# Optimization experiments

Hardware: AMD Instinct MI355X
Metric: run time of the kernel (lower is better)

## Reference

```python
import jax, jax.numpy as jnp
import numpy as np

B, C, H, W = 16, 256, 64, 64

def setup_inputs() -> dict:
    key = jax.random.key(0)
    ks = jax.random.split(key, 4)
    scale = 1.0 / np.sqrt(C)
    return {
        "x": jax.random.normal(ks[0], (B, C, H, W), dtype=jnp.float32),
        "w1": jax.random.normal(ks[1], (C, C), dtype=jnp.float32) * scale,
        "b1": jnp.zeros((C,), dtype=jnp.float32),
        "w2": jax.random.normal(ks[2], (C, C), dtype=jnp.float32) * scale,
        "b2": jnp.zeros((C,), dtype=jnp.float32),
        "w3": jax.random.normal(ks[3], (C, C), dtype=jnp.float32) * scale,
        "b3": jnp.zeros((C,), dtype=jnp.float32),
    }

def reference(x, w1, b1, w2, b2, w3, b3):
    b, c, h, w = x.shape
    n = h * w
    # 1x1 convs == per-pixel linear maps over channels; w has shape [C_out, C_in]
    def proj(wt, bias):
        return jnp.einsum('bchw,oc->bohw', x, wt) + bias[None, :, None, None]
    v = proj(w1, b1).reshape(b, c, n).transpose(0, 2, 1)   # [B, N, C]
    q = proj(w2, b2).reshape(b, c, n)                      # [B, C, N]
    k = proj(w3, b3).reshape(b, c, n)                      # [B, C, N]
    weight = jnp.einsum('bcn,bdn->bcd', q, k)              # [B, C, C]
    # global softmax over the entire flattened C*C matrix per batch element
    weight = jax.nn.softmax(weight.reshape(b, -1), axis=1).reshape(b, c, c)
    out = jnp.einsum('bnc,bcd->bdn', v, weight)            # [B, C, N]
    return out.reshape(x.shape)
```

## Files before the change

### kernel.cpp

```cpp
#include <hip/hip_runtime.h>


typedef unsigned short u16;
typedef __attribute__((ext_vector_type(8))) short short8;
typedef __attribute__((ext_vector_type(4))) float floatx4;

__device__ __forceinline__ u16 f2b(float f) {
  union { float f; unsigned int u; } v; v.f = f;
  unsigned int u = v.u;
  return (u16)((u + 0x7fffu + ((u >> 16) & 1u)) >> 16);
}
__device__ __forceinline__ float b2f(u16 h) {
  union { unsigned int u; float f; } v; v.u = ((unsigned int)h) << 16;
  return v.f;
}

__global__ __launch_bounds__(256) void prep_w_kernel(
    const float* __restrict__ w1, const float* __restrict__ w2, const float* __restrict__ w3,
    u16* __restrict__ W1Th, u16* __restrict__ W2h, u16* __restrict__ W2l,
    u16* __restrict__ W3h, u16* __restrict__ W3l) {
  const int blk = blockIdx.x, t = threadIdx.x;
  if (blk < 64) {
    __shared__ float tile[32][33];
    const int e0 = (blk & 7) * 32, c0 = (blk >> 3) * 32;
    const int tx = t & 31, ty = t >> 5;
#pragma unroll
    for (int i = 0; i < 4; ++i)
      tile[ty + i * 8][tx] = w1[(c0 + ty + i * 8) * 256 + e0 + tx];
    __syncthreads();
#pragma unroll
    for (int i = 0; i < 4; ++i)
      W1Th[(e0 + ty + i * 8) * 256 + c0 + tx] = f2b(tile[tx][ty + i * 8]);
  } else {
    const int i = (blk - 64) * 256 + t;
    const int e = i & 0xffff;
    const float f = (i >> 16) ? w3[e] : w2[e];
    u16 h = f2b(f);
    if (i >> 16) { W3h[e] = h; W3l[e] = f2b(f - b2f(h)); }
    else         { W2h[e] = h; W2l[e] = f2b(f - b2f(h)); }
  }
}

__device__ __forceinline__ void stage8(const float4 a, const float4 b,
                                       u16* dH, u16* dL, float& xa) {
  const float f[8] = {a.x, a.y, a.z, a.w, b.x, b.y, b.z, b.w};
  union { u16 h8[8]; uint4 q; } uh, ul;
#pragma unroll
  for (int i = 0; i < 8; ++i) {
    const u16 hi = f2b(f[i]);
    uh.h8[i] = hi;
    ul.h8[i] = f2b(f[i] - b2f(hi));
    xa += f[i];
  }
  *(uint4*)dH = uh.q;
  *(uint4*)dL = ul.q;
}

__global__ __launch_bounds__(512, 2) void gram_kernel(
    const float* __restrict__ x, float* __restrict__ Gp, float* __restrict__ xsum) {
  constexpr int LR = 40;
  __shared__ u16 lH[2][256 * LR], lL[2][256 * LR];
  const int b = blockIdx.x >> 4, s = blockIdx.x & 15;
  const float* Xb = x + (long)b * 1048576 + s * 256;
  const int t = threadIdx.x;
  const int lane = t & 63, wave = t >> 6;
  const int quad = lane >> 4, l16 = lane & 15;
  const int wm = (wave & 1) * 128, wn = (wave >> 1) * 64;
  const int r0 = t >> 2, qc = (t & 3) * 8;
  const int r1 = r0 + 128;
  floatx4 acc[8][4] = {};
  float xa0 = 0.f, xa1 = 0.f;
  float4 p[4];
  p[0] = *(const float4*)(Xb + (long)r0 * 4096 + qc);
  p[1] = *(const float4*)(Xb + (long)r0 * 4096 + qc + 4);
  p[2] = *(const float4*)(Xb + (long)r1 * 4096 + qc);
  p[3] = *(const float4*)(Xb + (long)r1 * 4096 + qc + 4);
  stage8(p[0], p[1], lH[0] + r0 * LR + qc, lL[0] + r0 * LR + qc, xa0);
  stage8(p[2], p[3], lH[0] + r1 * LR + qc, lL[0] + r1 * LR + qc, xa1);
  __syncthreads();
  for (int kb = 0; kb < 8; ++kb) {
    const int cur = kb & 1, nxt = cur ^ 1;
    if (kb < 7) {
      const long kk = (kb + 1) * 32;
      p[0] = *(const float4*)(Xb + (long)r0 * 4096 + kk + qc);
      p[1] = *(const float4*)(Xb + (long)r0 * 4096 + kk + qc + 4);
      p[2] = *(const float4*)(Xb + (long)r1 * 4096 + kk + qc);
      p[3] = *(const float4*)(Xb + (long)r1 * 4096 + kk + qc + 4);
    }
    const u16* cH = lH[cur];
    const u16* cL = lL[cur];
#pragma unroll
    for (int j = 0; j < 4; ++j) {
      const short8 bh = *(const short8*)(cH + (wn + j * 16 + l16) * LR + quad * 8);
      const short8 bl = *(const short8*)(cL + (wn + j * 16 + l16) * LR + quad * 8);
#pragma unroll
      for (int i = 0; i < 8; ++i) {
        const short8 ah = *(const short8*)(cH + (wm + i * 16 + l16) * LR + quad * 8);
        const short8 al = *(const short8*)(cL + (wm + i * 16 + l16) * LR + quad * 8);
        acc[i][j] = __builtin_amdgcn_mfma_f32_16x16x32_bf16(ah, bh, acc[i][j], 0, 0, 0);
        acc[i][j] = __builtin_amdgcn_mfma_f32_16x16x32_bf16(ah, bl, acc[i][j], 0, 0, 0);
        acc[i][j] = __builtin_amdgcn_mfma_f32_16x16x32_bf16(al, bh, acc[i][j], 0, 0, 0);
      }
    }
    if (kb < 7) {
      stage8(p[0], p[1], lH[nxt] + r0 * LR + qc, lL[nxt] + r0 * LR + qc, xa0);
      stage8(p[2], p[3], lH[nxt] + r1 * LR + qc, lL[nxt] + r1 * LR + qc, xa1);
    }
    __syncthreads();
  }
  {
    float v = xa0;
    v += __shfl_xor(v, 1);
    v += __shfl_xor(v, 2);
    if ((t & 3) == 0) atomicAdd(&xsum[b * 256 + r0], v);
    v = xa1;
    v += __shfl_xor(v, 1);
    v += __shfl_xor(v, 2);
    if ((t & 3) == 0) atomicAdd(&xsum[b * 256 + r1], v);
  }
  float* G = Gp + ((long)b * 16 + s) * 65536;
#pragma unroll
  for (int i = 0; i < 8; ++i) {
    const int row0 = wm + i * 16 + quad * 4;
#pragma unroll
    for (int j = 0; j < 4; ++j) {
      const int col = wn + j * 16 + l16;
#pragma unroll
      for (int r = 0; r < 4; ++r)
        G[(long)(row0 + r) * 256 + col] = acc[i][j][r];
    }
  }
}

__global__ void reduce_g_kernel(const float* __restrict__ Gp, u16* __restrict__ Gh,
                                u16* __restrict__ Gl) {
  const long e = (long)blockIdx.x * 256 + threadIdx.x;
  const long base = ((e >> 16) << 20) + (e & 65535);
  float s = 0.f;
#pragma unroll
  for (int i = 0; i < 16; ++i) s += Gp[base + (long)i * 65536];
  u16 h = f2b(s);
  Gh[e] = h;
  Gl[e] = f2b(s - b2f(h));
}

template <bool X3, int EPI>
__global__ __launch_bounds__(256) void gemm_small(
    const u16* __restrict__ Ah, const u16* __restrict__ Al,
    const u16* __restrict__ Bh, const u16* __restrict__ Bl,
    long aBatch, long bBatch, long oBatch,
    float* __restrict__ outF, u16* __restrict__ outH, u16* __restrict__ outL) {
  constexpr int LR = 40;
  __shared__ u16 smem[(X3 ? 4 : 2) * 64 * LR];
  u16* lAh = smem;
  u16* lBh = smem + 64 * LR;
  u16* lAl = X3 ? (smem + 2 * 64 * LR) : nullptr;
  u16* lBl = X3 ? (smem + 3 * 64 * LR) : nullptr;
  const int b = blockIdx.z;
  const int tm = blockIdx.x & 3, tn = blockIdx.x >> 2;
  const u16* Ahb = Ah + (long)b * aBatch + (long)tm * 64 * 256;
  const u16* Bhb = Bh + (long)b * bBatch + (long)tn * 64 * 256;
  const u16* Alb = X3 ? (Al + (long)b * aBatch + (long)tm * 64 * 256) : nullptr;
  const u16* Blb = X3 ? (Bl + (long)b * bBatch + (long)tn * 64 * 256) : nullptr;
  const int t = threadIdx.x;
  const int lane = t & 63, wave = t >> 6;
  const int quad = lane >> 4, l16 = lane & 15;
  const int wm = (wave & 1) * 32, wn = (wave >> 1) * 32;
  const int r = t >> 2, qc = (t & 3) * 8;
  floatx4 acc[2][2] = {};
  for (int kk = 0; kk < 256; kk += 32) {
    __syncthreads();
    *(uint4*)(lAh + r * LR + qc) = *(const uint4*)(Ahb + (long)r * 256 + kk + qc);
    *(uint4*)(lBh + r * LR + qc) = *(const uint4*)(Bhb + (long)r * 256 + kk + qc);
    if (X3) {
      *(uint4*)(lAl + r * LR + qc) = *(const uint4*)(Alb + (long)r * 256 + kk + qc);
      *(uint4*)(lBl + r * LR + qc) = *(const uint4*)(Blb + (long)r * 256 + kk + qc);
    }
    __syncthreads();
    short8 afh[2], bfh[2], afl[2], bfl[2];
#pragma unroll
    for (int i = 0; i < 2; ++i) {
      afh[i] = *(const short8*)(lAh + (wm + i * 16 + l16) * LR + quad * 8);
      bfh[i] = *(const short8*)(lBh + (wn + i * 16 + l16) * LR + quad * 8);
      if (X3) {
        afl[i] = *(const short8*)(lAl + (wm + i * 16 + l16) * LR + quad * 8);
        bfl[i] = *(const short8*)(lBl + (wn + i * 16 + l16) * LR + quad * 8);
      }
    }
#pragma unroll
    for (int i = 0; i < 2; ++i)
#pragma unroll
      for (int j = 0; j < 2; ++j) {
        acc[i][j] = __builtin_amdgcn_mfma_f32_16x16x32_bf16(afh[i], bfh[j], acc[i][j], 0, 0, 0);
        if (X3) {
          acc[i][j] = __builtin_amdgcn_mfma_f32_16x16x32_bf16(afh[i], bfl[j], acc[i][j], 0, 0, 0);
          acc[i][j] = __builtin_amdgcn_mfma_f32_16x16x32_bf16(afl[i], bfh[j], acc[i][j], 0, 0, 0);
        }
      }
  }
  const long obase = (long)b * oBatch;
#pragma unroll
  for (int i = 0; i < 2; ++i) {
    const int mb = tm * 64 + wm + i * 16 + quad * 4;
#pragma unroll
    for (int j = 0; j < 2; ++j) {
      const int n = tn * 64 + wn + j * 16 + l16;
#pragma unroll
      for (int rr = 0; rr < 4; ++rr) {
        const float v = acc[i][j][rr];
        const long idx = obase + (long)(mb + rr) * 256 + n;
        if (EPI == 0) {
          outF[idx] = v;
        } else if (EPI == 1) {
          u16 h = f2b(v);
          outH[idx] = h;
          outL[idx] = f2b(v - b2f(h));
        } else {
          outH[idx] = f2b(v);
        }
      }
    }
  }
}

__global__ __launch_bounds__(256) void gemm_out(
    const u16* __restrict__ Mh, const float* __restrict__ x,
    const float* __restrict__ bb, float* __restrict__ out) {
  constexpr int LR = 40;
  __shared__ u16 lA[128 * LR], lB[128 * LR];
  const int b = blockIdx.z;
  const int tm = blockIdx.x & 1, tn = blockIdx.x >> 1;
  const u16* Ab = Mh + (long)b * 65536;
  const float* Xb = x + (long)b * 1048576 + tn * 128;
  const int t = threadIdx.x;
  const int lane = t & 63, wave = t >> 6;
  const int quad = lane >> 4, l16 = lane & 15;
  const int wm = (wave & 1) * 64, wn = (wave >> 1) * 64;
  const int erp = (t >> 4) * 2;
  const int n0 = (t & 15) * 8;
  floatx4 acc[4][4] = {};
  for (int kk = 0; kk < 256; kk += 32) {
    __syncthreads();
#pragma unroll
    for (int h = 0; h < 2; ++h) {
      const int r = (t >> 2) + h * 64;
      *(uint4*)(lA + r * LR + (t & 3) * 8) =
          *(const uint4*)(Ab + (long)(tm * 128 + r) * 256 + kk + (t & 3) * 8);
    }
    {
      const float4 a0 = *(const float4*)(Xb + (long)(kk + erp) * 4096 + n0);
      const float4 a1 = *(const float4*)(Xb + (long)(kk + erp) * 4096 + n0 + 4);
      const float4 c0 = *(const float4*)(Xb + (long)(kk + erp + 1) * 4096 + n0);
      const float4 c1 = *(const float4*)(Xb + (long)(kk + erp + 1) * 4096 + n0 + 4);
      const float fa[8] = {a0.x, a0.y, a0.z, a0.w, a1.x, a1.y, a1.z, a1.w};
      const float fc[8] = {c0.x, c0.y, c0.z, c0.w, c1.x, c1.y, c1.z, c1.w};
#pragma unroll
      for (int i = 0; i < 8; ++i) {
        const int nl = n0 + i;
        const int sb = (erp >> 3) ^ ((nl >> 4) & 3);
        const unsigned int pk =
            (unsigned int)f2b(fa[i]) | ((unsigned int)f2b(fc[i]) << 16);
        *(unsigned int*)(lB + nl * LR + sb * 8 + (erp & 7)) = pk;
      }
    }
    __syncthreads();
    short8 af[4], bf[4];
#pragma unroll
    for (int i = 0; i < 4; ++i) {
      af[i] = *(const short8*)(lA + (wm + i * 16 + l16) * LR + quad * 8);
      const int n = wn + i * 16 + l16;
      const int rb = quad ^ ((n >> 4) & 3);
      bf[i] = *(const short8*)(lB + n * LR + rb * 8);
    }
#pragma unroll
    for (int i = 0; i < 4; ++i)
#pragma unroll
      for (int j = 0; j < 4; ++j)
        acc[i][j] = __builtin_amdgcn_mfma_f32_16x16x32_bf16(af[i], bf[j], acc[i][j], 0, 0, 0);
  }
  const long obase = (long)b * 1048576;
#pragma unroll
  for (int i = 0; i < 4; ++i) {
    const int mb = tm * 128 + wm + i * 16 + quad * 4;
#pragma unroll
    for (int j = 0; j < 4; ++j) {
      const int n = tn * 128 + wn + j * 16 + l16;
#pragma unroll
      for (int r = 0; r < 4; ++r)
        out[obase + (long)(mb + r) * 4096 + n] = acc[i][j][r] + bb[b * 256 + mb + r];
    }
  }
}

__global__ __launch_bounds__(512) void bias_prep_kernel(
    const float* __restrict__ w2, const float* __restrict__ w3,
    const float* __restrict__ xsum, float* __restrict__ S2, float* __restrict__ S3) {
  __shared__ float xs[256];
  const int b = blockIdx.x, t = threadIdx.x;
  if (t < 256) xs[t] = xsum[b * 256 + t];
  __syncthreads();
  const float* wm = (t < 256) ? w2 : w3;
  const int a = t & 255;
  float s = 0.f;
#pragma unroll 4
  for (int c = 0; c < 256; ++c) s += wm[a * 256 + c] * xs[c];
  if (t < 256) S2[b * 256 + a] = s;
  else         S3[b * 256 + a] = s;
}

__global__ __launch_bounds__(256) void softmax_pass1(
    const float* __restrict__ Lt, const float* __restrict__ S2, const float* __restrict__ S3,
    const float* __restrict__ b2, const float* __restrict__ b3,
    float* __restrict__ bm, float* __restrict__ bs) {
  __shared__ float ls2[256], lb2[256];
  __shared__ float redm[4], reds[4];
  const int b = blockIdx.y, blk = blockIdx.x, t = threadIdx.x;
  ls2[t] = S2[b * 256 + t];
  lb2[t] = b2[t];
  __syncthreads();
  const int fw0 = blk * 2048 + t * 8;
  const int d = fw0 >> 8, a0 = fw0 & 255;
  const float c1 = b3[d];
  const float c0 = S3[b * 256 + d] + 4096.f * c1;
  const long base = (long)b * 65536 + fw0;
  float4 v0 = *(const float4*)(Lt + base);
  float4 v1 = *(const float4*)(Lt + base + 4);
  float v[8] = {v0.x, v0.y, v0.z, v0.w, v1.x, v1.y, v1.z, v1.w};
  float m = -3.4e38f;
#pragma unroll
  for (int i = 0; i < 8; ++i) {
    v[i] += lb2[a0 + i] * c0 + c1 * ls2[a0 + i];
    m = fmaxf(m, v[i]);
  }
  for (int o = 32; o; o >>= 1) m = fmaxf(m, __shfl_xor(m, o));
  const int wid = t >> 6, lane = t & 63;
  if (lane == 0) redm[wid] = m;
  __syncthreads();
  const float bmax = fmaxf(fmaxf(redm[0], redm[1]), fmaxf(redm[2], redm[3]));
  float s = 0.f;
#pragma unroll
  for (int i = 0; i < 8; ++i) s += __expf(v[i] - bmax);
  for (int o = 32; o; o >>= 1) s += __shfl_xor(s, o);
  if (lane == 0) reds[wid] = s;
  __syncthreads();
  if (t == 0) {
    bm[b * 32 + blk] = bmax;
    bs[b * 32 + blk] = reds[0] + reds[1] + reds[2] + reds[3];
  }
}

__global__ __launch_bounds__(256) void softmax_pass3(
    const float* __restrict__ Lt, const float* __restrict__ S2, const float* __restrict__ S3,
    const float* __restrict__ b2, const float* __restrict__ b3,
    const float* __restrict__ bm, const float* __restrict__ bs,
    u16* __restrict__ WTh) {
  __shared__ float ls2[256], lb2[256];
  __shared__ float sM, sInv;
  const int b = blockIdx.y, blk = blockIdx.x, t = threadIdx.x;
  if (t < 64) {
    const float m = (t < 32) ? bm[b * 32 + t] : -3.4e38f;
    float s = (t < 32) ? bs[b * 32 + t] : 0.f;
    float M = m;
    for (int o = 32; o; o >>= 1) M = fmaxf(M, __shfl_xor(M, o));
    s *= __expf(m - M);
    for (int o = 32; o; o >>= 1) s += __shfl_xor(s, o);
    if (t == 0) { sM = M; sInv = 1.0f / s; }
  }
  ls2[t] = S2[b * 256 + t];
  lb2[t] = b2[t];
  __syncthreads();
  const float M = sM, inv = sInv;
  const int fw0 = blk * 2048 + t * 8;
  const int d = fw0 >> 8, a0 = fw0 & 255;
  const float c1 = b3[d];
  const float c0 = S3[b * 256 + d] + 4096.f * c1;
  const long base = (long)b * 65536 + fw0;
  float4 v0 = *(const float4*)(Lt + base);
  float4 v1 = *(const float4*)(Lt + base + 4);
  float v[8] = {v0.x, v0.y, v0.z, v0.w, v1.x, v1.y, v1.z, v1.w};
  union { u16 h[8]; uint4 q; } o;
#pragma unroll
  for (int i = 0; i < 8; ++i) {
    const float vv = v[i] + lb2[a0 + i] * c0 + c1 * ls2[a0 + i];
    o.h[i] = f2b(__expf(vv - M) * inv);
  }
  *(uint4*)(WTh + base) = o.q;
}

__global__ void bb_kernel(const u16* __restrict__ WTh, const float* __restrict__ b1,
                          float* __restrict__ bb) {
  const int b = blockIdx.x, d = threadIdx.x;
  const u16* row = WTh + (long)b * 65536 + d * 256;
  float s = 0.f;
#pragma unroll 4
  for (int c = 0; c < 256; ++c) s += b2f(row[c]) * b1[c];
  bb[b * 256 + d] = s;
}

extern "C" void kernel_launch(void* const* d_in, const int* in_sizes, int n_in,
                              void* d_out, int out_size, void* d_ws, size_t ws_size,
                              hipStream_t stream) {
  const float* x  = (const float*)d_in[0];
  const float* w1 = (const float*)d_in[1];
  const float* b1 = (const float*)d_in[2];
  const float* w2 = (const float*)d_in[3];
  const float* b2 = (const float*)d_in[4];
  const float* w3 = (const float*)d_in[5];
  const float* b3 = (const float*)d_in[6];
  float* out = (float*)d_out;

  char* ws = (char*)d_ws;
  size_t off = 0;
  auto alloc = [&](size_t bytes) {
    void* p = ws + off;
    off += (bytes + 255) & ~(size_t)255;
    return p;
  };
  float* Gp = (float*)alloc(16ull * 16 * 65536 * 4);
  u16* Gh   = (u16*)alloc(16ull * 65536 * 2);
  u16* Gl   = (u16*)alloc(16ull * 65536 * 2);
  u16* T3h  = (u16*)alloc(16ull * 65536 * 2);
  u16* T3l  = (u16*)alloc(16ull * 65536 * 2);
  float* Lb = (float*)alloc(16ull * 65536 * 4);
  u16* WTh  = (u16*)alloc(16ull * 65536 * 2);
  u16* Mh   = (u16*)alloc(16ull * 65536 * 2);
  u16* W1Th = (u16*)alloc(65536 * 2);
  u16* W2h  = (u16*)alloc(65536 * 2);
  u16* W2l  = (u16*)alloc(65536 * 2);
  u16* W3h  = (u16*)alloc(65536 * 2);
  u16* W3l  = (u16*)alloc(65536 * 2);
  float* xsum = (float*)alloc(16 * 256 * 4);
  float* S2   = (float*)alloc(16 * 256 * 4);
  float* S3   = (float*)alloc(16 * 256 * 4);
  float* bmx  = (float*)alloc(16 * 32 * 4);
  float* bsx  = (float*)alloc(16 * 32 * 4);
  float* bb   = (float*)alloc(16 * 256 * 4);

  hipMemsetAsync(xsum, 0, 16 * 256 * 4, stream);
  prep_w_kernel<<<576, 256, 0, stream>>>(w1, w2, w3, W1Th, W2h, W2l, W3h, W3l);

  gram_kernel<<<256, 512, 0, stream>>>(x, Gp, xsum);
  reduce_g_kernel<<<4096, 256, 0, stream>>>(Gp, Gh, Gl);

  gemm_small<true, 1><<<dim3(16, 1, 16), 256, 0, stream>>>(
      W3h, W3l, Gh, Gl, 0, 65536, 65536, nullptr, T3h, T3l);
  gemm_small<true, 0><<<dim3(16, 1, 16), 256, 0, stream>>>(
      T3h, T3l, W2h, W2l, 65536, 0, 65536, Lb, nullptr, nullptr);

  bias_prep_kernel<<<16, 512, 0, stream>>>(w2, w3, xsum, S2, S3);
  softmax_pass1<<<dim3(32, 16), 256, 0, stream>>>(Lb, S2, S3, b2, b3, bmx, bsx);
  softmax_pass3<<<dim3(32, 16), 256, 0, stream>>>(Lb, S2, S3, b2, b3, bmx, bsx, WTh);

  bb_kernel<<<16, 256, 0, stream>>>(WTh, b1, bb);
  gemm_small<false, 2><<<dim3(16, 1, 16), 256, 0, stream>>>(
      WTh, nullptr, W1Th, nullptr, 65536, 0, 65536, nullptr, Mh, nullptr);
  gemm_out<<<dim3(64, 1, 16), 256, 0, stream>>>(Mh, x, bb, out);
}
```

Measured before the change: 239.0 us.

## Atomically reduce Gram partials, fuse bias sum into softmax, widen gemm_out tile

The gram kernel now accumulates its split-K partial results straight into one fp32 Gram buffer with device-scope atomics, so the 16x partial buffer and its reduction pass go away. A light split kernel only converts the result to hi/lo bf16. The bias-mixing vector bb is computed inside softmax_pass3 with a warp shuffle reduction, which removes bb_kernel. gemm_out now covers all 256 output rows per block, so each block converts its x tile to bf16 once instead of twice, at the cost of more accumulator registers and fp32 atomic contention.

```diff
diff --git a/kernel.cpp b/kernel.cpp
--- a/kernel.cpp
+++ b/kernel.cpp
@@ -57,7 +57,7 @@
 }
 
 __global__ __launch_bounds__(512, 2) void gram_kernel(
-    const float* __restrict__ x, float* __restrict__ Gp, float* __restrict__ xsum) {
+    const float* __restrict__ x, float* __restrict__ Gf, float* __restrict__ xsum) {
   constexpr int LR = 40;
   __shared__ u16 lH[2][256 * LR], lL[2][256 * LR];
   const int b = blockIdx.x >> 4, s = blockIdx.x & 15;
@@ -118,7 +118,7 @@
     v += __shfl_xor(v, 2);
     if ((t & 3) == 0) atomicAdd(&xsum[b * 256 + r1], v);
   }
-  float* G = Gp + ((long)b * 16 + s) * 65536;
+  float* G = Gf + (long)b * 65536;
 #pragma unroll
   for (int i = 0; i < 8; ++i) {
     const int row0 = wm + i * 16 + quad * 4;
@@ -127,19 +127,17 @@
       const int col = wn + j * 16 + l16;
 #pragma unroll
       for (int r = 0; r < 4; ++r)
-        G[(long)(row0 + r) * 256 + col] = acc[i][j][r];
-    }
-  }
-}
-
-__global__ void reduce_g_kernel(const float* __restrict__ Gp, u16* __restrict__ Gh,
-                                u16* __restrict__ Gl) {
+        __hip_atomic_fetch_add(&G[(long)(row0 + r) * 256 + col], acc[i][j][r],
+                               __ATOMIC_RELAXED, __HIP_MEMORY_SCOPE_AGENT);
+    }
+  }
+}
+
+__global__ void split_g_kernel(const float* __restrict__ Gf, u16* __restrict__ Gh,
+                               u16* __restrict__ Gl) {
   const long e = (long)blockIdx.x * 256 + threadIdx.x;
-  const long base = ((e >> 16) << 20) + (e & 65535);
-  float s = 0.f;
-#pragma unroll
-  for (int i = 0; i < 16; ++i) s += Gp[base + (long)i * 65536];
-  u16 h = f2b(s);
+  const float s = Gf[e];
+  const u16 h = f2b(s);
   Gh[e] = h;
   Gl[e] = f2b(s - b2f(h));
 }
@@ -223,29 +221,29 @@
   }
 }
 
-__global__ __launch_bounds__(256) void gemm_out(
+__global__ __launch_bounds__(256, 2) void gemm_out(
     const u16* __restrict__ Mh, const float* __restrict__ x,
     const float* __restrict__ bb, float* __restrict__ out) {
   constexpr int LR = 40;
-  __shared__ u16 lA[128 * LR], lB[128 * LR];
+  __shared__ u16 lA[256 * LR], lB[128 * LR];
   const int b = blockIdx.z;
-  const int tm = blockIdx.x & 1, tn = blockIdx.x >> 1;
+  const int tn = blockIdx.x;
   const u16* Ab = Mh + (long)b * 65536;
   const float* Xb = x + (long)b * 1048576 + tn * 128;
   const int t = threadIdx.x;
   const int lane = t & 63, wave = t >> 6;
   const int quad = lane >> 4, l16 = lane & 15;
-  const int wm = (wave & 1) * 64, wn = (wave >> 1) * 64;
+  const int wm = wave * 64;
   const int erp = (t >> 4) * 2;
   const int n0 = (t & 15) * 8;
-  floatx4 acc[4][4] = {};
+  floatx4 acc[4][8] = {};
   for (int kk = 0; kk < 256; kk += 32) {
     __syncthreads();
 #pragma unroll
-    for (int h = 0; h < 2; ++h) {
+    for (int h = 0; h < 4; ++h) {
       const int r = (t >> 2) + h * 64;
       *(uint4*)(lA + r * LR + (t & 3) * 8) =
-          *(const uint4*)(Ab + (long)(tm * 128 + r) * 256 + kk + (t & 3) * 8);
+          *(const uint4*)(Ab + (long)r * 256 + kk + (t & 3) * 8);
     }
     {
       const float4 a0 = *(const float4*)(Xb + (long)(kk + erp) * 4096 + n0);
@@ -264,27 +262,29 @@
       }
     }
     __syncthreads();
-    short8 af[4], bf[4];
-#pragma unroll
-    for (int i = 0; i < 4; ++i) {
+    short8 af[4], bf[8];
+#pragma unroll
+    for (int j = 0; j < 8; ++j) {
+      const int n = j * 16 + l16;
+      const int rb = quad ^ ((n >> 4) & 3);
+      bf[j] = *(const short8*)(lB + n * LR + rb * 8);
+    }
+#pragma unroll
+    for (int i = 0; i < 4; ++i)
       af[i] = *(const short8*)(lA + (wm + i * 16 + l16) * LR + quad * 8);
-      const int n = wn + i * 16 + l16;
-      const int rb = quad ^ ((n >> 4) & 3);
-      bf[i] = *(const short8*)(lB + n * LR + rb * 8);
-    }
 #pragma unroll
     for (int i = 0; i < 4; ++i)
 #pragma unroll
-      for (int j = 0; j < 4; ++j)
+      for (int j = 0; j < 8; ++j)
         acc[i][j] = __builtin_amdgcn_mfma_f32_16x16x32_bf16(af[i], bf[j], acc[i][j], 0, 0, 0);
   }
   const long obase = (long)b * 1048576;
 #pragma unroll
   for (int i = 0; i < 4; ++i) {
-    const int mb = tm * 128 + wm + i * 16 + quad * 4;
-#pragma unroll
-    for (int j = 0; j < 4; ++j) {
-      const int n = tn * 128 + wn + j * 16 + l16;
+    const int mb = wm + i * 16 + quad * 4;
+#pragma unroll
+    for (int j = 0; j < 8; ++j) {
+      const int n = tn * 128 + j * 16 + l16;
 #pragma unroll
       for (int r = 0; r < 4; ++r)
         out[obase + (long)(mb + r) * 4096 + n] = acc[i][j][r] + bb[b * 256 + mb + r];
@@ -353,8 +353,8 @@
     const float* __restrict__ Lt, const float* __restrict__ S2, const float* __restrict__ S3,
     const float* __restrict__ b2, const float* __restrict__ b3,
     const float* __restrict__ bm, const float* __restrict__ bs,
-    u16* __restrict__ WTh) {
-  __shared__ float ls2[256], lb2[256];
+    const float* __restrict__ b1, u16* __restrict__ WTh, float* __restrict__ bb) {
+  __shared__ float ls2[256], lb2[256], lb1[256];
   __shared__ float sM, sInv;
   const int b = blockIdx.y, blk = blockIdx.x, t = threadIdx.x;
   if (t < 64) {
@@ -368,6 +368,7 @@
   }
   ls2[t] = S2[b * 256 + t];
   lb2[t] = b2[t];
+  lb1[t] = b1[t];
   __syncthreads();
   const float M = sM, inv = sInv;
   const int fw0 = blk * 2048 + t * 8;
@@ -379,22 +380,17 @@
   float4 v1 = *(const float4*)(Lt + base + 4);
   float v[8] = {v0.x, v0.y, v0.z, v0.w, v1.x, v1.y, v1.z, v1.w};
   union { u16 h[8]; uint4 q; } o;
+  float bsum = 0.f;
 #pragma unroll
   for (int i = 0; i < 8; ++i) {
     const float vv = v[i] + lb2[a0 + i] * c0 + c1 * ls2[a0 + i];
-    o.h[i] = f2b(__expf(vv - M) * inv);
+    const float w = __expf(vv - M) * inv;
+    o.h[i] = f2b(w);
+    bsum += w * lb1[a0 + i];
   }
   *(uint4*)(WTh + base) = o.q;
-}
-
-__global__ void bb_kernel(const u16* __restrict__ WTh, const float* __restrict__ b1,
-                          float* __restrict__ bb) {
-  const int b = blockIdx.x, d = threadIdx.x;
-  const u16* row = WTh + (long)b * 65536 + d * 256;
-  float s = 0.f;
-#pragma unroll 4
-  for (int c = 0; c < 256; ++c) s += b2f(row[c]) * b1[c];
-  bb[b * 256 + d] = s;
+  for (int off = 16; off; off >>= 1) bsum += __shfl_xor(bsum, off);
+  if ((t & 31) == 0) bb[b * 256 + d] = bsum;
 }
 
 extern "C" void kernel_launch(void* const* d_in, const int* in_sizes, int n_in,
@@ -416,7 +412,8 @@
     off += (bytes + 255) & ~(size_t)255;
     return p;
   };
-  float* Gp = (float*)alloc(16ull * 16 * 65536 * 4);
+  float* Gf   = (float*)alloc(16ull * 65536 * 4);
+  float* xsum = (float*)alloc(16 * 256 * 4);
   u16* Gh   = (u16*)alloc(16ull * 65536 * 2);
   u16* Gl   = (u16*)alloc(16ull * 65536 * 2);
   u16* T3h  = (u16*)alloc(16ull * 65536 * 2);
@@ -429,18 +426,17 @@
   u16* W2l  = (u16*)alloc(65536 * 2);
   u16* W3h  = (u16*)alloc(65536 * 2);
   u16* W3l  = (u16*)alloc(65536 * 2);
-  float* xsum = (float*)alloc(16 * 256 * 4);
   float* S2   = (float*)alloc(16 * 256 * 4);
   float* S3   = (float*)alloc(16 * 256 * 4);
   float* bmx  = (float*)alloc(16 * 32 * 4);
   float* bsx  = (float*)alloc(16 * 32 * 4);
   float* bb   = (float*)alloc(16 * 256 * 4);
 
-  hipMemsetAsync(xsum, 0, 16 * 256 * 4, stream);
+  hipMemsetAsync(Gf, 0, 16ull * 65536 * 4 + 16 * 256 * 4, stream);
   prep_w_kernel<<<576, 256, 0, stream>>>(w1, w2, w3, W1Th, W2h, W2l, W3h, W3l);
 
-  gram_kernel<<<256, 512, 0, stream>>>(x, Gp, xsum);
-  reduce_g_kernel<<<4096, 256, 0, stream>>>(Gp, Gh, Gl);
+  gram_kernel<<<256, 512, 0, stream>>>(x, Gf, xsum);
+  split_g_kernel<<<4096, 256, 0, stream>>>(Gf, Gh, Gl);
 
   gemm_small<true, 1><<<dim3(16, 1, 16), 256, 0, stream>>>(
       W3h, W3l, Gh, Gl, 0, 65536, 65536, nullptr, T3h, T3l);
@@ -449,10 +445,10 @@
 
   bias_prep_kernel<<<16, 512, 0, stream>>>(w2, w3, xsum, S2, S3);
   softmax_pass1<<<dim3(32, 16), 256, 0, stream>>>(Lb, S2, S3, b2, b3, bmx, bsx);
-  softmax_pass3<<<dim3(32, 16), 256, 0, stream>>>(Lb, S2, S3, b2, b3, bmx, bsx, WTh);
-
-  bb_kernel<<<16, 256, 0, stream>>>(WTh, b1, bb);
+  softmax_pass3<<<dim3(32, 16), 256, 0, stream>>>(Lb, S2, S3, b2, b3, bmx, bsx,
+                                                  b1, WTh, bb);
+
   gemm_small<false, 2><<<dim3(16, 1, 16), 256, 0, stream>>>(
       WTh, nullptr, W1Th, nullptr, 65536, 0, 65536, nullptr, Mh, nullptr);
-  gemm_out<<<dim3(64, 1, 16), 256, 0, stream>>>(Mh, x, bb, out);
-}
+  gemm_out<<<dim3(32, 1, 16), 256, 0, stream>>>(Mh, x, bb, out);
+}
```

New measurement: 253.4 us. +6.1%, slower.
